# Optimization experiments

Hardware: AMD Instinct MI355X
Metric: run time of the kernel (lower is better)

The kernel has to match this reference:

```python
import jax, jax.numpy as jnp
import numpy as np

NUM_HEADS = 12

def setup_inputs() -> dict:
    key = jax.random.key(0)
    k1, k2, k3, k4 = jax.random.split(key, 4)
    B, N, C = 64, 197, 768
    x = jax.random.normal(k1, (B, N, C), dtype=jnp.float32)
    w_qkv = jax.random.normal(k2, (3 * C, C), dtype=jnp.float32) * (C ** -0.5)
    w_proj = jax.random.normal(k3, (C, C), dtype=jnp.float32) * (C ** -0.5)
    b_proj = jax.random.normal(k4, (C,), dtype=jnp.float32) * 0.01
    return {"x": x, "w_qkv": w_qkv, "w_proj": w_proj, "b_proj": b_proj}

def reference(x, w_qkv, w_proj, b_proj):
    B, N, C = x.shape
    H = NUM_HEADS
    hd = C // H
    scale = hd ** -0.5
    # qkv linear (no bias): [B,N,3C] -> [3,B,H,N,hd]
    qkv = jnp.einsum('bnc,dc->bnd', x, w_qkv).reshape(B, N, 3, H, hd)
    qkv = jnp.transpose(qkv, (2, 0, 3, 1, 4))
    q, k, v = qkv[0], qkv[1], qkv[2]
    # full attention matrix [B,H,N,N] (materialized, matching the original)
    attn = jax.nn.softmax(jnp.einsum('bhnd,bhmd->bhnm', q, k) * scale, axis=-1)
    # CLS-token attention stats: mean over heads of attn row 0 (patch tokens) -> [B, N-1]
    global_attn = jnp.mean(attn[:, :, 0, 1:], axis=1)
    out = jnp.einsum('bhnm,bhmd->bhnd', attn, v)          # [B,H,N,hd]
    out = jnp.transpose(out, (0, 2, 1, 3)).reshape(B, N, C)
    out = jnp.einsum('bnc,dc->bnd', out, w_proj) + b_proj
    return out, global_attn
```

## Files before the change

kernel.cpp:

```cpp
#include <hip/hip_runtime.h>
#include <math.h>

#define B_   64
#define N_   197
#define C_   768
#define H_   12
#define HD_  64
#define BH_  (B_ * H_)
#define M_   (B_ * N_)

typedef _Float16 half8 __attribute__((ext_vector_type(8)));
typedef _Float16 half4 __attribute__((ext_vector_type(4)));
typedef float    f32x4 __attribute__((ext_vector_type(4)));

#define XH_OFF   0u
#define WQH_OFF  19365888u
#define WPH_OFF  22904832u
#define QH_OFF   24084480u
#define KH_OFF   43450368u
#define VH_OFF   62816256u
#define OH_OFF   82182144u
#define P0_OFF   101548032u
#define WS_BYTES 102150144u

__device__ __forceinline__ half8 h8zero() {
    half8 z;
    #pragma unroll
    for (int i = 0; i < 8; ++i) z[i] = (_Float16)0;
    return z;
}

__device__ __forceinline__ void async16(const _Float16* g, _Float16* l) {
    __builtin_amdgcn_global_load_lds(
        (const __attribute__((address_space(1))) void*)g,
        (__attribute__((address_space(3))) void*)l,
        16, 0, 0);
}

__device__ __forceinline__ int xcd_swz(int i, int nwg) {
    const int q = nwg >> 3, r = nwg & 7;
    const int xcd = i & 7, j = i >> 3;
    return (xcd < r ? xcd * (q + 1) : r * (q + 1) + (xcd - r) * q) + j;
}

__global__ void k_ws_too_small(float* out, float ws_bytes) { out[0] = -ws_bytes; }

__global__ __launch_bounds__(256) void k_cvt_all(const float* __restrict__ x,
                                                 const float* __restrict__ wq,
                                                 const float* __restrict__ wp,
                                                 _Float16* __restrict__ Xh,
                                                 _Float16* __restrict__ Wqh,
                                                 _Float16* __restrict__ Wph) {
    int i = blockIdx.x * blockDim.x + threadIdx.x;
    const float* src;
    _Float16*    dst;
    if (i < 1210368)      { src = x;  dst = Xh; }
    else if (i < 1431552) { src = wq; dst = Wqh; i -= 1210368; }
    else                  { src = wp; dst = Wph; i -= 1431552; }
    float4 f0 = *(const float4*)(src + (size_t)i * 8);
    float4 f1 = *(const float4*)(src + (size_t)i * 8 + 4);
    half8 h;
    h[0]=(_Float16)f0.x; h[1]=(_Float16)f0.y; h[2]=(_Float16)f0.z; h[3]=(_Float16)f0.w;
    h[4]=(_Float16)f1.x; h[5]=(_Float16)f1.y; h[6]=(_Float16)f1.z; h[7]=(_Float16)f1.w;
    *(half8*)(dst + (size_t)i * 8) = h;
}

__device__ __forceinline__ void mfma_nt_core_256(const _Float16* __restrict__ A,
                                                 const _Float16* __restrict__ B,
                                                 int M, int K, int m0, int n0,
                                                 _Float16* As, _Float16* Bs,
                                                 f32x4 (&acc)[8][4]) {
    const int tid  = threadIdx.x;
    const int lane = tid & 63;
    const int w    = tid >> 6;
    const int wm   = w >> 2, wn = w & 3;
    const int ln   = lane & 15, kq = lane >> 4;

    const int srow = tid >> 3;
    const int kcs  = (((tid & 7) ^ (srow & 7)) << 3);
    int ra00 = m0 +       srow; if (ra00 >= M) ra00 = 0;
    int ra01 = m0 +  64 + srow; if (ra01 >= M) ra01 = 0;
    int ra10 = m0 + 128 + srow; if (ra10 >= M) ra10 = 0;
    int ra11 = m0 + 192 + srow; if (ra11 >= M) ra11 = 0;
    const _Float16* A00 = A + (size_t)ra00 * K + kcs;
    const _Float16* A01 = A + (size_t)ra01 * K + kcs;
    const _Float16* A10 = A + (size_t)ra10 * K + kcs;
    const _Float16* A11 = A + (size_t)ra11 * K + kcs;
    const _Float16* B00 = B + (size_t)(n0 +       srow) * K + kcs;
    const _Float16* B01 = B + (size_t)(n0 +  64 + srow) * K + kcs;
    const _Float16* B10 = B + (size_t)(n0 + 128 + srow) * K + kcs;
    const _Float16* B11 = B + (size_t)(n0 + 192 + srow) * K + kcs;
    const int dOff = w << 9;

    const int kx    = (ln & 7) << 3;
    const int aBase = wm * 8192 + ln * 64;
    const int bBase = (wn >> 1) * 8192 + (wn & 1) * 4096 + ln * 64;

    half8 af[4][2], bf[4][2];

    async16(A00, As + dOff);          async16(A01, As + 4096 + dOff);
    async16(A10, As + 8192 + dOff);   async16(A11, As + 12288 + dOff);
    async16(B00, Bs + dOff);          async16(B01, Bs + 4096 + dOff);
    async16(B10, Bs + 8192 + dOff);   async16(B11, Bs + 12288 + dOff);

    const int NT = K >> 6;
    #pragma unroll 1
    for (int t = 0; t < NT; ++t) {
        const int cur  = (t & 1) << 14;
        const int nb   = 16384 - cur;
        const int koff = (t + 1) << 6;
        const bool pre = (t + 1 < NT);
        const _Float16* Ac = As + cur;
        const _Float16* Bc = Bs + cur;

        if (pre) {
            async16(A00 + koff, As + nb + dOff);
            async16(A01 + koff, As + nb + 4096 + dOff);
            async16(A10 + koff, As + nb + 8192 + dOff);
            async16(A11 + koff, As + nb + 12288 + dOff);
            asm volatile("s_waitcnt vmcnt(4)" ::: "memory");
        } else {
            asm volatile("s_waitcnt vmcnt(0)" ::: "memory");
        }
        __builtin_amdgcn_s_barrier();
        __builtin_amdgcn_sched_barrier(0);
        #pragma unroll
        for (int m4 = 0; m4 < 4; ++m4)
            #pragma unroll
            for (int kk = 0; kk < 2; ++kk)
                af[m4][kk] = *(const half8*)&Ac[aBase + m4 * 1024 + ((kk * 32 + kq * 8) ^ kx)];
        #pragma unroll
        for (int n2 = 0; n2 < 2; ++n2)
            #pragma unroll
            for (int kk = 0; kk < 2; ++kk)
                bf[n2][kk] = *(const half8*)&Bc[bBase + n2 * 1024 + ((kk * 32 + kq * 8) ^ kx)];
        __builtin_amdgcn_s_setprio(1);
        #pragma unroll
        for (int m4 = 0; m4 < 4; ++m4)
            #pragma unroll
            for (int n2 = 0; n2 < 2; ++n2)
                #pragma unroll
                for (int kk = 0; kk < 2; ++kk)
                    acc[m4][n2] = __builtin_amdgcn_mfma_f32_16x16x32_f16(af[m4][kk], bf[n2][kk], acc[m4][n2], 0, 0, 0);
        __builtin_amdgcn_s_setprio(0);
        __builtin_amdgcn_sched_barrier(0);
        __builtin_amdgcn_s_barrier();

        if (pre) {
            async16(B00 + koff, Bs + nb + dOff);
            async16(B01 + koff, Bs + nb + 4096 + dOff);
        }
        #pragma unroll
        for (int n2 = 0; n2 < 2; ++n2)
            #pragma unroll
            for (int kk = 0; kk < 2; ++kk)
                bf[2 + n2][kk] = *(const half8*)&Bc[bBase + (2 + n2) * 1024 + ((kk * 32 + kq * 8) ^ kx)];
        __builtin_amdgcn_s_setprio(1);
        #pragma unroll
        for (int m4 = 0; m4 < 4; ++m4)
            #pragma unroll
            for (int n2 = 0; n2 < 2; ++n2)
                #pragma unroll
                for (int kk = 0; kk < 2; ++kk)
                    acc[m4][2 + n2] = __builtin_amdgcn_mfma_f32_16x16x32_f16(af[m4][kk], bf[2 + n2][kk], acc[m4][2 + n2], 0, 0, 0);
        __builtin_amdgcn_s_setprio(0);
        __builtin_amdgcn_sched_barrier(0);
        __builtin_amdgcn_s_barrier();

        if (pre) {
            async16(B10 + koff, Bs + nb + 8192 + dOff);
            async16(B11 + koff, Bs + nb + 12288 + dOff);
        }
        #pragma unroll
        for (int m4 = 0; m4 < 4; ++m4)
            #pragma unroll
            for (int kk = 0; kk < 2; ++kk)
                af[m4][kk] = *(const half8*)&Ac[aBase + (4 + m4) * 1024 + ((kk * 32 + kq * 8) ^ kx)];
        __builtin_amdgcn_s_setprio(1);
        #pragma unroll
        for (int m4 = 0; m4 < 4; ++m4)
            #pragma unroll
            for (int n2 = 0; n2 < 2; ++n2)
                #pragma unroll
                for (int kk = 0; kk < 2; ++kk)
                    acc[4 + m4][n2] = __builtin_amdgcn_mfma_f32_16x16x32_f16(af[m4][kk], bf[n2][kk], acc[4 + m4][n2], 0, 0, 0);
        __builtin_amdgcn_s_setprio(0);
        __builtin_amdgcn_sched_barrier(0);
        __builtin_amdgcn_s_barrier();

        __builtin_amdgcn_s_setprio(1);
        #pragma unroll
        for (int m4 = 0; m4 < 4; ++m4)
            #pragma unroll
            for (int n2 = 0; n2 < 2; ++n2)
                #pragma unroll
                for (int kk = 0; kk < 2; ++kk)
                    acc[4 + m4][2 + n2] = __builtin_amdgcn_mfma_f32_16x16x32_f16(af[m4][kk], bf[2 + n2][kk], acc[4 + m4][2 + n2], 0, 0, 0);
        __builtin_amdgcn_s_setprio(0);
        asm volatile("s_waitcnt lgkmcnt(0)" ::: "memory");
        __builtin_amdgcn_sched_barrier(0);
        __builtin_amdgcn_s_barrier();
    }
}

__device__ __forceinline__ void mfma_nt_core_h(const _Float16* __restrict__ A,
                                               const _Float16* __restrict__ B,
                                               int M, int K, int m0, int n0,
                                               _Float16* As, _Float16* Bs,
                                               f32x4 (&acc)[4][4]) {
    const int tid  = threadIdx.x;
    const int wave = tid >> 6, lane = tid & 63;
    const int wr   = (wave >> 1) << 6;
    const int wc   = (wave & 1) << 6;
    const int ln   = lane & 15, kq = lane >> 4;

    const int row0 = tid >> 2;
    const int ch0  = (tid & 3) << 3;
    int ar0 = m0 + row0;        if (ar0 >= M) ar0 = 0;
    int ar1 = m0 + 64 + row0;   if (ar1 >= M) ar1 = 0;
    const _Float16* A0 = A + (size_t)ar0 * K + ch0;
    const _Float16* A1 = A + (size_t)ar1 * K + ch0;
    const _Float16* B0 = B + (size_t)(n0 + row0) * K + ch0;
    const _Float16* B1 = B + (size_t)(n0 + 64 + row0) * K + ch0;
    _Float16* AsD = As + (wave << 9);
    _Float16* BsD = Bs + (wave << 9);

    async16(A0, AsD);        async16(A1, AsD + 2048);
    async16(B0, BsD);        async16(B1, BsD + 2048);
    __syncthreads();

    int cur = 0;
    for (int k0 = 0; k0 < K; k0 += 32) {
        const int nxt = cur ^ 1;
        if (k0 + 32 < K) {
            const int nb = nxt << 12;
            async16(A0 + k0 + 32, AsD + nb);
            async16(A1 + k0 + 32, AsD + nb + 2048);
            async16(B0 + k0 + 32, BsD + nb);
            async16(B1 + k0 + 32, BsD + nb + 2048);
        }
        const _Float16* Ac = As + (cur << 12);
        const _Float16* Bc = Bs + (cur << 12);
        half8 af[4], bf[4];
        #pragma unroll
        for (int t = 0; t < 4; ++t) {
            af[t] = *(const half8*)&Ac[(wr + t * 16 + ln) * 32 + kq * 8];
            bf[t] = *(const half8*)&Bc[(wc + t * 16 + ln) * 32 + kq * 8];
        }
        #pragma unroll
        for (int i = 0; i < 4; ++i)
            #pragma unroll
            for (int j = 0; j < 4; ++j)
                acc[i][j] = __builtin_amdgcn_mfma_f32_16x16x32_f16(af[i], bf[j], acc[i][j], 0, 0, 0);
        __syncthreads();
        cur = nxt;
    }
}

__global__ __launch_bounds__(512, 2) void k_qkv_mfma(const _Float16* __restrict__ Xh,
                                                     const _Float16* __restrict__ Wq,
                                                     _Float16* __restrict__ Qh,
                                                     _Float16* __restrict__ Kh,
                                                     _Float16* __restrict__ Vh) {
    __shared__ _Float16 As[32768];
    __shared__ _Float16 Bs[32768];
    const int work = xcd_swz(blockIdx.x, 50 * 9);
    const int m0 = (work / 9) << 8;
    const int n0 = (work % 9) << 8;
    f32x4 acc[8][4] = {};
    mfma_nt_core_256(Xh, Wq, M_, C_, m0, n0, As, Bs, acc);

    const int lane = threadIdx.x & 63;
    const int w    = threadIdx.x >> 6;
    const int wm = w >> 2, wn = w & 3;
    const int ln = lane & 15, kq = lane >> 4;

    _Float16* basep[4];
    float     scl[4];
    #pragma unroll
    for (int ni = 0; ni < 4; ++ni) {
        const int d  = n0 + wn * 64 + ni * 16 + ln;
        const int t3 = d / C_;
        const int rr = d - t3 * C_;
        const int h  = rr >> 6;
        const int e  = rr & 63;
        _Float16* tp = (t3 == 0) ? Qh : (t3 == 1) ? Kh : Vh;
        basep[ni] = tp + (size_t)h * N_ * HD_ + e;
        scl[ni]   = (t3 == 0) ? 0.125f : 1.f;
    }
    #pragma unroll
    for (int mi = 0; mi < 8; ++mi) {
        #pragma unroll
        for (int i = 0; i < 4; ++i) {
            const int m = m0 + wm * 128 + mi * 16 + kq * 4 + i;
            if (m >= M_) continue;
            const int b = m / N_;
            const int n = m - b * N_;
            const size_t rowoff = ((size_t)b * H_ * N_ + n) * HD_;
            #pragma unroll
            for (int ni = 0; ni < 4; ++ni)
                basep[ni][rowoff] = (_Float16)(acc[mi][ni][i] * scl[ni]);
        }
    }
}

__global__ __launch_bounds__(256) void k_proj_mfma(const _Float16* __restrict__ Oh,
                                                   const _Float16* __restrict__ Wp,
                                                   const float* __restrict__ bias,
                                                   float* __restrict__ out) {
    __shared__ _Float16 As[2 * 4096];
    __shared__ _Float16 Bs[2 * 4096];
    const int work = xcd_swz(blockIdx.y * 6 + blockIdx.x, 6 * 99);
    const int m0 = (work / 6) << 7;
    const int n0 = (work % 6) << 7;
    f32x4 acc[4][4] = {};
    mfma_nt_core_h(Oh, Wp, M_, C_, m0, n0, As, Bs, acc);

    const int lane = threadIdx.x & 63;
    const int wave = threadIdx.x >> 6;
    const int wr = (wave >> 1) << 6, wc = (wave & 1) << 6;
    const int ln = lane & 15, kq = lane >> 4;
    float bv[4];
    #pragma unroll
    for (int nt = 0; nt < 4; ++nt) bv[nt] = bias[n0 + wc + nt * 16 + ln];
    #pragma unroll
    for (int mt = 0; mt < 4; ++mt) {
        #pragma unroll
        for (int i = 0; i < 4; ++i) {
            const int m = m0 + wr + mt * 16 + kq * 4 + i;
            if (m >= M_) continue;
            #pragma unroll
            for (int nt = 0; nt < 4; ++nt)
                out[(size_t)m * C_ + n0 + wc + nt * 16 + ln] = acc[mt][nt][i] + bv[nt];
        }
    }
}

__global__ __launch_bounds__(256, 3) void k_attn(const _Float16* __restrict__ Qh,
                                                 const _Float16* __restrict__ Kh,
                                                 const _Float16* __restrict__ Vh,
                                                 _Float16* __restrict__ Oh,
                                                 float* __restrict__ P0) {
    __shared__ _Float16 lds[27136];
    _Float16* Ks = lds;
    _Float16* Vt = lds + 13312;

    const int bh = blockIdx.x;
    const int b = bh / H_, h = bh - b * H_;
    const int tid = threadIdx.x, wave = tid >> 6, lane = tid & 63;
    const int ln = lane & 15, kq = lane >> 4;
    const size_t kvb = (size_t)bh * N_ * HD_;

    for (int idx = tid; idx < 208 * 8; idx += 256) {
        const int key = idx >> 3, c8 = idx & 7;
        half8 v = (key < N_) ? *(const half8*)(Kh + kvb + (size_t)key * HD_ + c8 * 8) : h8zero();
        *(half8*)&Ks[key * 64 + ((c8 ^ (key & 7)) << 3)] = v;
    }
    for (int idx = tid; idx < 197 * 8; idx += 256) {
        const int key = idx >> 3, c = (idx & 7) << 3;
        half8 v = *(const half8*)(Vh + kvb + (size_t)key * HD_ + c);
        #pragma unroll
        for (int j = 0; j < 8; ++j) Vt[(c + j) * 216 + key] = v[j];
    }
    for (int idx = tid; idx < 64 * 19; idx += 256) {
        const int d = idx / 19, k = 197 + (idx - d * 19);
        Vt[d * 216 + k] = (_Float16)0;
    }
    __syncthreads();

    const int swz = ln & 7;

    for (int rt = 0; rt < 4; ++rt) {
        if (rt * 64 + wave * 16 >= N_) continue;

        const int qrow = rt * 64 + wave * 16 + ln;
        const _Float16* Qp = Qh + kvb + (size_t)((qrow < N_) ? qrow : 0) * HD_ + kq * 8;
        half8 qf0 = *(const half8*)Qp;
        half8 qf1 = *(const half8*)(Qp + 32);

        f32x4 acc[13] = {};
        __builtin_amdgcn_s_setprio(1);
        #pragma unroll
        for (int c = 0; c < 13; ++c) {
            const _Float16* kp = &Ks[(c * 16 + ln) * 64];
            half8 kf0 = *(const half8*)(kp + ((kq ^ swz) << 3));
            half8 kf1 = *(const half8*)(kp + (((4 + kq) ^ swz) << 3));
            acc[c] = __builtin_amdgcn_mfma_f32_16x16x32_f16(kf0, qf0, acc[c], 0, 0, 0);
            acc[c] = __builtin_amdgcn_mfma_f32_16x16x32_f16(kf1, qf1, acc[c], 0, 0, 0);
        }
        __builtin_amdgcn_s_setprio(0);

        float m = -1e30f;
        #pragma unroll
        for (int c = 0; c < 12; ++c)
            #pragma unroll
            for (int r = 0; r < 4; ++r) m = fmaxf(m, acc[c][r]);
        #pragma unroll
        for (int r = 0; r < 4; ++r) {
            float x = (kq * 4 + r < 5) ? acc[12][r] : -1e30f;
            acc[12][r] = x;
            m = fmaxf(m, x);
        }
        m = fmaxf(m, __shfl_xor(m, 16));
        m = fmaxf(m, __shfl_xor(m, 32));
        float s = 0.f;
        #pragma unroll
        for (int c = 0; c < 13; ++c)
            #pragma unroll
            for (int r = 0; r < 4; ++r) {
                float e = __expf(acc[c][r] - m);
                acc[c][r] = e;
                s += e;
            }
        s += __shfl_xor(s, 16);
        s += __shfl_xor(s, 32);
        const float inv = 1.f / s;

        if (rt == 0 && wave == 0 && ln == 0) {
            #pragma unroll
            for (int c = 0; c < 13; ++c)
                #pragma unroll
                for (int r = 0; r < 4; ++r) {
                    const int key = c * 16 + kq * 4 + r;
                    if (key >= 1 && key < N_)
                        P0[(size_t)bh * 196 + key - 1] = acc[c][r] * inv;
                }
        }

        f32x4 o4[4] = {};
        __builtin_amdgcn_s_setprio(1);
        #pragma unroll
        for (int u = 0; u < 13; ++u) {
            half4 af;
            af[0] = (_Float16)(acc[u][0] * inv);
            af[1] = (_Float16)(acc[u][1] * inv);
            af[2] = (_Float16)(acc[u][2] * inv);
            af[3] = (_Float16)(acc[u][3] * inv);
            #pragma unroll
            for (int n = 0; n < 4; ++n) {
                half4 bf = *(const half4*)&Vt[(n * 16 + ln) * 216 + u * 16 + kq * 4];
                o4[n] = __builtin_amdgcn_mfma_f32_16x16x16f16(af, bf, o4[n], 0, 0, 0);
            }
        }
        __builtin_amdgcn_s_setprio(0);

        const int g0 = rt * 64 + wave * 16 + kq * 4;
        #pragma unroll
        for (int r = 0; r < 4; ++r) {
            const int g = g0 + r;
            if (g >= N_) continue;
            _Float16* op = Oh + ((size_t)b * N_ + g) * C_ + h * HD_;
            #pragma unroll
            for (int n = 0; n < 4; ++n) op[n * 16 + ln] = (_Float16)o4[n][r];
        }
    }
}

__global__ void k_gattn(const float* __restrict__ P0, float* __restrict__ out2) {
    const int idx = blockIdx.x * blockDim.x + threadIdx.x;
    const int b = idx / (N_ - 1), m = idx - b * (N_ - 1);
    float s = 0.f;
    #pragma unroll
    for (int h = 0; h < H_; ++h) s += P0[((size_t)(b * H_ + h)) * 196 + m];
    out2[idx] = s * (1.f / H_);
}

extern "C" void kernel_launch(void* const* d_in, const int* in_sizes, int n_in,
                              void* d_out, int out_size, void* d_ws, size_t ws_size,
                              hipStream_t stream) {
    const float* x      = (const float*)d_in[0];
    const float* w_qkv  = (const float*)d_in[1];
    const float* w_proj = (const float*)d_in[2];
    const float* b_proj = (const float*)d_in[3];
    float* out = (float*)d_out;
    char* ws   = (char*)d_ws;

    if (ws_size < (size_t)WS_BYTES) {
        k_ws_too_small<<<1, 1, 0, stream>>>(out, (float)ws_size);
        return;
    }

    _Float16* Xh  = (_Float16*)(ws + XH_OFF);
    _Float16* Wqh = (_Float16*)(ws + WQH_OFF);
    _Float16* Wph = (_Float16*)(ws + WPH_OFF);
    _Float16* Qh  = (_Float16*)(ws + QH_OFF);
    _Float16* Kh  = (_Float16*)(ws + KH_OFF);
    _Float16* Vh  = (_Float16*)(ws + VH_OFF);
    _Float16* Oh  = (_Float16*)(ws + OH_OFF);
    float*    P0  = (float*)   (ws + P0_OFF);

    k_cvt_all<<<5880, 256, 0, stream>>>(x, w_qkv, w_proj, Xh, Wqh, Wph);

    k_qkv_mfma <<<dim3(450),   512, 0, stream>>>(Xh, Wqh, Qh, Kh, Vh);
    k_attn     <<<dim3(BH_),   256, 0, stream>>>(Qh, Kh, Vh, Oh, P0);
    k_gattn    <<<dim3(49),    256, 0, stream>>>(P0, out + (size_t)M_ * C_);
    k_proj_mfma<<<dim3(6, 99), 256, 0, stream>>>(Oh, Wph, b_proj, out);
}
```

Baseline: 220.6 us.

## Switch QKV GEMM mainloop to 3-stage BK=32 async pipeline

Replaces the double-buffered BK=64 mainloop, which interleaved partial loads and MFMAs across four barrier phases, with a triple-buffered BK=32 ring. Each iteration loads all A/B fragments, runs 32 MFMAs, then issues the async copy for tile t+3. The XOR swizzle and staging layout are recomputed for 32-wide rows, and shared memory per buffer is reduced. This aims to hide global latency with deeper prefetch and simpler scheduling, at the cost of more barriers per unit of K and the loss of the fine-grained interleaving and setprio hints.

```diff
diff --git a/kernel.cpp b/kernel.cpp
--- a/kernel.cpp
+++ b/kernel.cpp
@@ -76,130 +76,66 @@
     const int wm   = w >> 2, wn = w & 3;
     const int ln   = lane & 15, kq = lane >> 4;
 
-    const int srow = tid >> 3;
-    const int kcs  = (((tid & 7) ^ (srow & 7)) << 3);
-    int ra00 = m0 +       srow; if (ra00 >= M) ra00 = 0;
-    int ra01 = m0 +  64 + srow; if (ra01 >= M) ra01 = 0;
-    int ra10 = m0 + 128 + srow; if (ra10 >= M) ra10 = 0;
-    int ra11 = m0 + 192 + srow; if (ra11 >= M) ra11 = 0;
-    const _Float16* A00 = A + (size_t)ra00 * K + kcs;
-    const _Float16* A01 = A + (size_t)ra01 * K + kcs;
-    const _Float16* A10 = A + (size_t)ra10 * K + kcs;
-    const _Float16* A11 = A + (size_t)ra11 * K + kcs;
-    const _Float16* B00 = B + (size_t)(n0 +       srow) * K + kcs;
-    const _Float16* B01 = B + (size_t)(n0 +  64 + srow) * K + kcs;
-    const _Float16* B10 = B + (size_t)(n0 + 128 + srow) * K + kcs;
-    const _Float16* B11 = B + (size_t)(n0 + 192 + srow) * K + kcs;
+    const int srow = tid >> 2;
+    const int kcs  = (((tid & 3) ^ ((tid >> 3) & 3)) << 3);
+    int ra0 = m0 +       srow; if (ra0 >= M) ra0 = 0;
+    int ra1 = m0 + 128 + srow; if (ra1 >= M) ra1 = 0;
+    const _Float16* A0 = A + (size_t)ra0 * K + kcs;
+    const _Float16* A1 = A + (size_t)ra1 * K + kcs;
+    const _Float16* B0 = B + (size_t)(n0 +       srow) * K + kcs;
+    const _Float16* B1 = B + (size_t)(n0 + 128 + srow) * K + kcs;
     const int dOff = w << 9;
 
-    const int kx    = (ln & 7) << 3;
-    const int aBase = wm * 8192 + ln * 64;
-    const int bBase = (wn >> 1) * 8192 + (wn & 1) * 4096 + ln * 64;
-
-    half8 af[4][2], bf[4][2];
-
-    async16(A00, As + dOff);          async16(A01, As + 4096 + dOff);
-    async16(A10, As + 8192 + dOff);   async16(A11, As + 12288 + dOff);
-    async16(B00, Bs + dOff);          async16(B01, Bs + 4096 + dOff);
-    async16(B10, Bs + 8192 + dOff);   async16(B11, Bs + 12288 + dOff);
-
-    const int NT = K >> 6;
+    const int rdx   = ((kq ^ ((ln >> 1) & 3)) << 3);
+    const int aBase = wm * 4096 + ln * 32;
+    const int bBase = wn * 2048 + ln * 32;
+
+    #pragma unroll
+    for (int p = 0; p < 3; ++p) {
+        const int koff = p << 5;
+        _Float16* dA = As + p * 8192 + dOff;
+        _Float16* dB = Bs + p * 8192 + dOff;
+        async16(A0 + koff, dA);   async16(A1 + koff, dA + 4096);
+        async16(B0 + koff, dB);   async16(B1 + koff, dB + 4096);
+    }
+
+    const int NT = K >> 5;
+    int cur = 0;
     #pragma unroll 1
     for (int t = 0; t < NT; ++t) {
-        const int cur  = (t & 1) << 14;
-        const int nb   = 16384 - cur;
-        const int koff = (t + 1) << 6;
-        const bool pre = (t + 1 < NT);
-        const _Float16* Ac = As + cur;
-        const _Float16* Bc = Bs + cur;
-
-        if (pre) {
-            async16(A00 + koff, As + nb + dOff);
-            async16(A01 + koff, As + nb + 4096 + dOff);
-            async16(A10 + koff, As + nb + 8192 + dOff);
-            async16(A11 + koff, As + nb + 12288 + dOff);
-            asm volatile("s_waitcnt vmcnt(4)" ::: "memory");
-        } else {
-            asm volatile("s_waitcnt vmcnt(0)" ::: "memory");
-        }
+        if (t < NT - 2)       asm volatile("s_waitcnt vmcnt(8)" ::: "memory");
+        else if (t == NT - 2) asm volatile("s_waitcnt vmcnt(4)" ::: "memory");
+        else                  asm volatile("s_waitcnt vmcnt(0)" ::: "memory");
         __builtin_amdgcn_s_barrier();
         __builtin_amdgcn_sched_barrier(0);
-        #pragma unroll
-        for (int m4 = 0; m4 < 4; ++m4)
-            #pragma unroll
-            for (int kk = 0; kk < 2; ++kk)
-                af[m4][kk] = *(const half8*)&Ac[aBase + m4 * 1024 + ((kk * 32 + kq * 8) ^ kx)];
-        #pragma unroll
-        for (int n2 = 0; n2 < 2; ++n2)
-            #pragma unroll
-            for (int kk = 0; kk < 2; ++kk)
-                bf[n2][kk] = *(const half8*)&Bc[bBase + n2 * 1024 + ((kk * 32 + kq * 8) ^ kx)];
-        __builtin_amdgcn_s_setprio(1);
-        #pragma unroll
-        for (int m4 = 0; m4 < 4; ++m4)
-            #pragma unroll
-            for (int n2 = 0; n2 < 2; ++n2)
-                #pragma unroll
-                for (int kk = 0; kk < 2; ++kk)
-                    acc[m4][n2] = __builtin_amdgcn_mfma_f32_16x16x32_f16(af[m4][kk], bf[n2][kk], acc[m4][n2], 0, 0, 0);
-        __builtin_amdgcn_s_setprio(0);
-        __builtin_amdgcn_sched_barrier(0);
-        __builtin_amdgcn_s_barrier();
-
-        if (pre) {
-            async16(B00 + koff, Bs + nb + dOff);
-            async16(B01 + koff, Bs + nb + 4096 + dOff);
-        }
-        #pragma unroll
-        for (int n2 = 0; n2 < 2; ++n2)
-            #pragma unroll
-            for (int kk = 0; kk < 2; ++kk)
-                bf[2 + n2][kk] = *(const half8*)&Bc[bBase + (2 + n2) * 1024 + ((kk * 32 + kq * 8) ^ kx)];
-        __builtin_amdgcn_s_setprio(1);
-        #pragma unroll
-        for (int m4 = 0; m4 < 4; ++m4)
-            #pragma unroll
-            for (int n2 = 0; n2 < 2; ++n2)
-                #pragma unroll
-                for (int kk = 0; kk < 2; ++kk)
-                    acc[m4][2 + n2] = __builtin_amdgcn_mfma_f32_16x16x32_f16(af[m4][kk], bf[2 + n2][kk], acc[m4][2 + n2], 0, 0, 0);
-        __builtin_amdgcn_s_setprio(0);
-        __builtin_amdgcn_sched_barrier(0);
-        __builtin_amdgcn_s_barrier();
-
-        if (pre) {
-            async16(B10 + koff, Bs + nb + 8192 + dOff);
-            async16(B11 + koff, Bs + nb + 12288 + dOff);
-        }
-        #pragma unroll
-        for (int m4 = 0; m4 < 4; ++m4)
-            #pragma unroll
-            for (int kk = 0; kk < 2; ++kk)
-                af[m4][kk] = *(const half8*)&Ac[aBase + (4 + m4) * 1024 + ((kk * 32 + kq * 8) ^ kx)];
-        __builtin_amdgcn_s_setprio(1);
-        #pragma unroll
-        for (int m4 = 0; m4 < 4; ++m4)
-            #pragma unroll
-            for (int n2 = 0; n2 < 2; ++n2)
-                #pragma unroll
-                for (int kk = 0; kk < 2; ++kk)
-                    acc[4 + m4][n2] = __builtin_amdgcn_mfma_f32_16x16x32_f16(af[m4][kk], bf[n2][kk], acc[4 + m4][n2], 0, 0, 0);
-        __builtin_amdgcn_s_setprio(0);
-        __builtin_amdgcn_sched_barrier(0);
-        __builtin_amdgcn_s_barrier();
-
-        __builtin_amdgcn_s_setprio(1);
-        #pragma unroll
-        for (int m4 = 0; m4 < 4; ++m4)
-            #pragma unroll
-            for (int n2 = 0; n2 < 2; ++n2)
-                #pragma unroll
-                for (int kk = 0; kk < 2; ++kk)
-                    acc[4 + m4][2 + n2] = __builtin_amdgcn_mfma_f32_16x16x32_f16(af[m4][kk], bf[2 + n2][kk], acc[4 + m4][2 + n2], 0, 0, 0);
-        __builtin_amdgcn_s_setprio(0);
+
+        const _Float16* Ac = As + cur * 8192;
+        const _Float16* Bc = Bs + cur * 8192;
+        half8 af[8], bf[4];
+        #pragma unroll
+        for (int m4 = 0; m4 < 8; ++m4)
+            af[m4] = *(const half8*)&Ac[aBase + m4 * 512 + rdx];
+        #pragma unroll
+        for (int n2 = 0; n2 < 4; ++n2)
+            bf[n2] = *(const half8*)&Bc[bBase + n2 * 512 + rdx];
+        #pragma unroll
+        for (int m4 = 0; m4 < 8; ++m4)
+            #pragma unroll
+            for (int n2 = 0; n2 < 4; ++n2)
+                acc[m4][n2] = __builtin_amdgcn_mfma_f32_16x16x32_f16(af[m4], bf[n2], acc[m4][n2], 0, 0, 0);
+
         asm volatile("s_waitcnt lgkmcnt(0)" ::: "memory");
         __builtin_amdgcn_sched_barrier(0);
         __builtin_amdgcn_s_barrier();
+
+        if (t + 3 < NT) {
+            const int koff = (t + 3) << 5;
+            _Float16* dA = As + cur * 8192 + dOff;
+            _Float16* dB = Bs + cur * 8192 + dOff;
+            async16(A0 + koff, dA);   async16(A1 + koff, dA + 4096);
+            async16(B0 + koff, dB);   async16(B1 + koff, dB + 4096);
+        }
+        cur = (cur == 2) ? 0 : cur + 1;
     }
 }
 
@@ -262,8 +198,8 @@
                                                      _Float16* __restrict__ Qh,
                                                      _Float16* __restrict__ Kh,
                                                      _Float16* __restrict__ Vh) {
-    __shared__ _Float16 As[32768];
-    __shared__ _Float16 Bs[32768];
+    __shared__ _Float16 As[24576];
+    __shared__ _Float16 Bs[24576];
     const int work = xcd_swz(blockIdx.x, 50 * 9);
     const int m0 = (work / 9) << 8;
     const int n0 = (work % 9) << 8;
```

Result: no change. 224.6 us (+1.8%).
